# Optimization experiments

Measured on AMD Instinct MI355X. Metric: run time of the kernel, lower is better.

Reference implementation:

```python
import jax, jax.numpy as jnp
import numpy as np

S = 64        # memory_slots
SLOT_DIM = 256
BOND = 32     # bond_dim
NQ = 8        # num_qubits = max(4, ceil(log2(slot_dim)))
QDIM = 2 ** NQ  # 256
DIM = 1024    # input feature dim


def setup_inputs() -> dict:
    key = jax.random.key(0)
    ks = jax.random.split(key, 8)
    std = 1.0 / np.sqrt(BOND)
    x = jax.random.normal(ks[0], (8, 4096, DIM), dtype=jnp.float32)
    Wq = jax.random.normal(ks[1], (DIM, QDIM), dtype=jnp.float32) * 0.02
    bq = jnp.zeros((QDIM,), dtype=jnp.float32)
    Wd = jax.random.normal(ks[2], (SLOT_DIM, DIM), dtype=jnp.float32) * 0.02
    bd = jnp.zeros((DIM,), dtype=jnp.float32)
    # MPS cores batched over slots; original shapes per slot:
    #   q=0: (1,2,BOND), q=1..NQ-2: (BOND,2,BOND), q=NQ-1: (BOND,2,1)
    core_first = jax.random.normal(ks[3], (S, 2, BOND), dtype=jnp.float32) * std
    core_mid = jax.random.normal(ks[4], (S, NQ - 2, BOND, 2, BOND), dtype=jnp.float32) * std
    core_last = jax.random.normal(ks[5], (S, BOND, 2), dtype=jnp.float32) * std
    return {"x": x, "Wq": Wq, "bq": bq, "Wd": Wd, "bd": bd,
            "core_first": core_first, "core_mid": core_mid, "core_last": core_last}


def _amp_means(qa):
    """Per-qubit strided means of query amplitudes. qa: [b, 2^NQ] -> (m0, m1): [b, NQ]."""
    m0s, m1s = [], []
    for q in range(NQ):
        stride = 2 ** (NQ - q - 1)
        idx0 = np.arange(stride) * (2 * stride)  # qa[:, ::2*stride][:, :stride]
        idx1 = idx0 + stride                     # qa[:, stride::2*stride][:, :stride]
        m0s.append(qa[:, idx0].mean(axis=-1))
        m1s.append(qa[:, idx1].mean(axis=-1))
    return jnp.stack(m0s, axis=1), jnp.stack(m1s, axis=1)


def reference(x, Wq, bq, Wd, bd, core_first, core_mid, core_last):
    # x: [b, t, d]
    x_summary = x.mean(axis=1)                         # [b, d]
    qa = jax.nn.softmax(x_summary @ Wq + bq, axis=-1)  # [b, QDIM]
    m0, m1 = _amp_means(qa)                            # [b, NQ] each

    # MPS contraction, vectorized over (batch b, slot s)
    # q = 0: left bond is 1 -> result directly [b, S, BOND]
    res = (m0[:, 0, None, None] * core_first[None, :, 0, :]
           + m1[:, 0, None, None] * core_first[None, :, 1, :])
    for q in range(1, NQ - 1):
        wc = (m0[:, q, None, None, None] * core_mid[None, :, q - 1, :, 0, :]
              + m1[:, q, None, None, None] * core_mid[None, :, q - 1, :, 1, :])  # [b,S,B,B]
        res = jnp.einsum('bsl,bslr->bsr', res, wc)
    # q = NQ-1: right bond is 1
    wc_last = (m0[:, NQ - 1, None, None] * core_last[None, :, :, 0]
               + m1[:, NQ - 1, None, None] * core_last[None, :, :, 1])  # [b,S,B]
    overlaps = jnp.einsum('bsl,bsl->bs', res, wc_last)  # [b, S]

    attention = jax.nn.softmax(overlaps, axis=-1)       # [b, S]

    # read values: per-slot per-qubit core means, tiled to slot_dim
    f0 = core_first.mean(axis=(1, 2))                   # [S]
    fm = core_mid.mean(axis=(2, 3, 4))                  # [S, NQ-2]
    fl = core_last.mean(axis=(1, 2))                    # [S]
    feats = jnp.concatenate([f0[:, None], fm, fl[:, None]], axis=1)  # [S, NQ]
    rep = SLOT_DIM // NQ + 1
    slot_values = jnp.tile(feats, (1, rep))[:, :SLOT_DIM]            # [S, SLOT_DIM]

    read_out = attention @ slot_values                  # [b, SLOT_DIM]
    read_proj = read_out @ Wd + bd                      # [b, DIM]
    return x + read_proj[:, None, :]
```

## Files before the change

### kernel.cpp

```cpp
#include <hip/hip_runtime.h>
#include <hip/hip_bf16.h>

#define B_    8
#define T_    4096
#define D_    1024
#define S_    64
#define NQ_   8
#define QDIM_ 256
#define TB_   64
#define NTC_  (T_/TB_)
#define NMID  64

typedef __attribute__((ext_vector_type(4))) unsigned short u16x4;
typedef __attribute__((ext_vector_type(8))) unsigned short u16x8;
typedef __attribute__((ext_vector_type(4))) float f32x4;

__device__ __forceinline__ float b2f(unsigned short u) {
    union { unsigned int i; float f; } v; v.i = ((unsigned int)u) << 16; return v.f;
}
__device__ __forceinline__ unsigned short f2b(float f) {
    __hip_bfloat16 h = __float2bfloat16(f);
    return *reinterpret_cast<unsigned short*>(&h);
}

__device__ __forceinline__ float blockSum(float v, float* buf) {
    int tid = threadIdx.x;
    buf[tid] = v; __syncthreads();
    #pragma unroll
    for (int s = 128; s > 0; s >>= 1) { if (tid < s) buf[tid] += buf[tid + s]; __syncthreads(); }
    float r = buf[0]; __syncthreads();
    return r;
}
__device__ __forceinline__ float blockMax(float v, float* buf) {
    int tid = threadIdx.x;
    buf[tid] = v; __syncthreads();
    #pragma unroll
    for (int s = 128; s > 0; s >>= 1) { if (tid < s) buf[tid] = fmaxf(buf[tid], buf[tid + s]); __syncthreads(); }
    float r = buf[0]; __syncthreads();
    return r;
}

__device__ __forceinline__ bool detect_f32(const unsigned short* __restrict__ p,
                                           unsigned elo, unsigned ehi, int* cnt) {
    int tid = threadIdx.x;
    if (tid == 0) *cnt = 0;
    __syncthreads();
    unsigned short u = p[tid];
    unsigned e = (u >> 7) & 0xFF;
    bool ok = ((u & 0x7FFF) == 0) || (e >= elo && e <= ehi);
    unsigned long long bm = __ballot(ok);
    if ((tid & 63) == 0) atomicAdd(cnt, (int)__popcll(bm));
    __syncthreads();
    bool isf32 = (*cnt < 200);
    __syncthreads();
    return isf32;
}

__device__ __forceinline__ void gbar(int* slot, int target) {
    __syncthreads();
    if (threadIdx.x == 0) {
        __hip_atomic_fetch_add(slot, 1, __ATOMIC_RELEASE, __HIP_MEMORY_SCOPE_AGENT);
        while (__hip_atomic_load(slot, __ATOMIC_RELAXED, __HIP_MEMORY_SCOPE_AGENT) < target)
            __builtin_amdgcn_s_sleep(4);
        (void)__hip_atomic_load(slot, __ATOMIC_ACQUIRE, __HIP_MEMORY_SCOPE_AGENT);
    }
    __syncthreads();
}

__global__ __launch_bounds__(256)
void k_colsum(const void* __restrict__ x, float* __restrict__ partials) {
    __shared__ int cnt;
    bool xf32 = detect_f32((const unsigned short*)x, 100, 130, &cnt);
    int blk = blockIdx.x;
    int b  = blk >> 6;
    int tc = blk & 63;
    int tid = threadIdx.x;
    size_t base = ((size_t)(b * T_ + tc * TB_)) * D_ + tid * 4;
    float a0 = 0.f, a1 = 0.f, a2 = 0.f, a3 = 0.f;
    if (xf32) {
        const float* px = (const float*)x + base;
        #pragma unroll 8
        for (int i = 0; i < TB_; ++i) {
            f32x4 v = *reinterpret_cast<const f32x4*>(px + (size_t)i * D_);
            a0 += v[0]; a1 += v[1]; a2 += v[2]; a3 += v[3];
        }
    } else {
        const unsigned short* px = (const unsigned short*)x + base;
        #pragma unroll 8
        for (int i = 0; i < TB_; ++i) {
            u16x4 v = *reinterpret_cast<const u16x4*>(px + (size_t)i * D_);
            a0 += b2f(v[0]); a1 += b2f(v[1]); a2 += b2f(v[2]); a3 += b2f(v[3]);
        }
    }
    float* dst = partials + ((size_t)(tc * B_ + b)) * D_ + tid * 4;
    f32x4 r; r[0] = a0; r[1] = a1; r[2] = a2; r[3] = a3;
    *reinterpret_cast<f32x4*>(dst) = r;
}

struct MpsSh {
    float lcm[6 * 2048];
    float lcf[64];
    float lcl[64];
    float res[8][33];
    float nres[8][33];
    float lm0[64], lm1[64];
    float buf[256];
};
struct LogitsSh { float xs2[256]; float xs[128]; };
struct SmSh     { float qa[QDIM_]; float buf[256]; };
struct AttSh    { float att[S_]; float g[NQ_]; };
union Sh { MpsSh mps; LogitsSh lg; SmSh sm; AttSh att; };

__global__ __launch_bounds__(256)
void k_mid(const void* __restrict__ Wq, const void* __restrict__ bq,
           const void* __restrict__ Wd, const void* __restrict__ bd,
           const void* __restrict__ cf, const void* __restrict__ cm,
           const void* __restrict__ cl,
           const float* __restrict__ partials, float* __restrict__ plog,
           float* __restrict__ sm0m, float* __restrict__ sm1m,
           float* __restrict__ feats, float* __restrict__ ovl,
           float* __restrict__ read_proj, float* __restrict__ wdred,
           int* __restrict__ bar) {
    __shared__ Sh u;
    __shared__ int cnt;
    const int blk = blockIdx.x;
    const int tid = threadIdx.x;
    bool wf32 = detect_f32((const unsigned short*)Wq, 96, 126, &cnt);

    {
        int b = blk >> 3, dc = blk & 7;
        int d0 = dc * 128;
        float a = 0.f;
        for (int tc = (tid >> 7); tc < NTC_; tc += 2)
            a += partials[((size_t)(tc * B_ + b)) * D_ + d0 + (tid & 127)];
        u.lg.xs2[tid] = a;
        __syncthreads();
        if (tid < 128) u.lg.xs[tid] = (u.lg.xs2[tid] + u.lg.xs2[tid + 128]) * (1.f / (float)T_);
        __syncthreads();
        float lg = 0.f;
        if (wf32) {
            const float* w = (const float*)Wq + (size_t)d0 * QDIM_ + tid;
            #pragma unroll 8
            for (int d = 0; d < 128; ++d) lg += u.lg.xs[d] * w[(size_t)d * QDIM_];
        } else {
            const unsigned short* w = (const unsigned short*)Wq + (size_t)d0 * QDIM_ + tid;
            #pragma unroll 8
            for (int d = 0; d < 128; ++d) lg += u.lg.xs[d] * b2f(w[(size_t)d * QDIM_]);
        }
        plog[((size_t)(b * 8 + dc)) * QDIM_ + tid] = lg;
        if (tid < 128) {
            int flat = blk * 128 + tid;
            int j = flat >> 10, d = flat & (D_ - 1);
            float s = 0.f;
            if (wf32) {
                const float* w = (const float*)Wd;
                #pragma unroll 8
                for (int k = 0; k < 32; ++k) s += w[(size_t)(j + 8 * k) * D_ + d];
            } else {
                const unsigned short* w = (const unsigned short*)Wd;
                #pragma unroll 8
                for (int k = 0; k < 32; ++k) s += b2f(w[(size_t)(j + 8 * k) * D_ + d]);
            }
            wdred[flat] = s;
        }
    }
    gbar(bar + 0, NMID);

    if (blk < 8) {
        int b = blk;
        float lg = wf32 ? ((const float*)bq)[tid] : b2f(((const unsigned short*)bq)[tid]);
        for (int dc = 0; dc < 8; ++dc) lg += plog[((size_t)(b * 8 + dc)) * QDIM_ + tid];
        float mx = blockMax(lg, u.sm.buf);
        float e = __expf(lg - mx);
        float ss = blockSum(e, u.sm.buf);
        u.sm.qa[tid] = e / ss;
        __syncthreads();
        if (tid < 16) {
            int q = tid >> 1, bit = tid & 1;
            int sw = 1 << (7 - q);
            float acc = 0.f;
            for (int i = 0; i < sw; ++i) {
                int idx = 2 * sw * i + bit * sw;
                if (idx > QDIM_ - 1) idx = QDIM_ - 1;
                acc += u.sm.qa[idx];
            }
            float m = acc / (float)sw;
            if (bit == 0) sm0m[b * 8 + q] = m; else sm1m[b * 8 + q] = m;
        }
    }
    gbar(bar + 1, NMID);

    {
        int s = blk;
        MpsSh& M = u.mps;
        if (wf32) {
            const float* pcm = (const float*)cm + (size_t)s * 12288;
            for (int i = tid; i < 12288; i += 256) M.lcm[i] = pcm[i];
            if (tid < 64) {
                M.lcf[tid] = ((const float*)cf)[s * 64 + tid];
                M.lcl[tid] = ((const float*)cl)[s * 64 + tid];
            }
        } else {
            const unsigned short* pcm = (const unsigned short*)cm + (size_t)s * 12288;
            for (int i = tid; i < 12288; i += 256) M.lcm[i] = b2f(pcm[i]);
            if (tid < 64) {
                M.lcf[tid] = b2f(((const unsigned short*)cf)[s * 64 + tid]);
                M.lcl[tid] = b2f(((const unsigned short*)cl)[s * 64 + tid]);
            }
        }
        if (tid < 64) { M.lm0[tid] = sm0m[tid]; M.lm1[tid] = sm1m[tid]; }
        __syncthreads();

        {
            float v = (tid < 64) ? M.lcf[tid] : 0.f;
            float f0 = blockSum(v, M.buf) * (1.f / 64.f);
            float fj[6];
            for (int j = 0; j < 6; ++j) {
                float a = 0.f;
                for (int k = tid; k < 2048; k += 256) a += M.lcm[j * 2048 + k];
                fj[j] = blockSum(a, M.buf) * (1.f / 2048.f);
            }
            float w = (tid < 64) ? M.lcl[tid] : 0.f;
            float fl = blockSum(w, M.buf) * (1.f / 64.f);
            if (tid == 0) {
                feats[s * 8 + 0] = f0;
                #pragma unroll
                for (int j = 0; j < 6; ++j) feats[s * 8 + 1 + j] = fj[j];
                feats[s * 8 + 7] = fl;
            }
        }

        int b = tid >> 5, r = tid & 31;
        M.res[b][r] = M.lm0[b * 8 + 0] * M.lcf[r] + M.lm1[b * 8 + 0] * M.lcf[32 + r];
        __syncthreads();
        for (int q = 1; q <= 6; ++q) {
            float m0 = M.lm0[b * 8 + q], m1 = M.lm1[b * 8 + q];
            const float* C = &M.lcm[(q - 1) * 2048];
            float acc = 0.f;
            #pragma unroll 8
            for (int l = 0; l < 32; ++l)
                acc += M.res[b][l] * (m0 * C[l * 64 + r] + m1 * C[l * 64 + 32 + r]);
            M.nres[b][r] = acc;
            __syncthreads();
            M.res[b][r] = M.nres[b][r];
            __syncthreads();
        }
        {
            float m0 = M.lm0[b * 8 + 7], m1 = M.lm1[b * 8 + 7];
            float p = M.res[b][r] * (m0 * M.lcl[r * 2] + m1 * M.lcl[r * 2 + 1]);
            #pragma unroll
            for (int off = 16; off > 0; off >>= 1) p += __shfl_xor(p, off, 64);
            if (r == 0) ovl[b * 64 + s] = p;
        }
    }
    gbar(bar + 2, NMID);

    if (blk < 8) {
        int b = blk;
        if (tid < 64) {
            float o = ovl[b * 64 + tid];
            float mx = o;
            #pragma unroll
            for (int off = 32; off > 0; off >>= 1) mx = fmaxf(mx, __shfl_xor(mx, off, 64));
            float e = __expf(o - mx);
            float se = e;
            #pragma unroll
            for (int off = 32; off > 0; off >>= 1) se += __shfl_xor(se, off, 64);
            u.att.att[tid] = e / se;
        }
        __syncthreads();
        if (tid < 8) {
            float g = 0.f;
            for (int s2 = 0; s2 < S_; ++s2) g += u.att.att[s2] * feats[s2 * 8 + tid];
            u.att.g[tid] = g;
        }
        __syncthreads();
        #pragma unroll
        for (int i = 0; i < 4; ++i) {
            int d = tid + i * 256;
            float a = wf32 ? ((const float*)bd)[d] : b2f(((const unsigned short*)bd)[d]);
            #pragma unroll
            for (int j = 0; j < 8; ++j) a += u.att.g[j] * wdred[(size_t)j * D_ + d];
            read_proj[(size_t)b * D_ + d] = a;
        }
    }
}

__global__ __launch_bounds__(256)
void k_add(const void* __restrict__ x, const float* __restrict__ rp,
           void* __restrict__ out) {
    __shared__ int cnt;
    bool xf32 = detect_f32((const unsigned short*)x, 100, 130, &cnt);
    size_t base = (((size_t)blockIdx.x) * 256 + threadIdx.x) * 8;
    int b = (int)(base >> 22);
    int d = (int)(base & (D_ - 1));
    const float* r = rp + (size_t)b * D_ + d;
    f32x4 r0 = *reinterpret_cast<const f32x4*>(r);
    f32x4 r1 = *reinterpret_cast<const f32x4*>(r + 4);
    if (xf32) {
        const float* px = (const float*)x + base;
        f32x4 v0 = *reinterpret_cast<const f32x4*>(px);
        f32x4 v1 = *reinterpret_cast<const f32x4*>(px + 4);
        f32x4 o0 = v0 + r0;
        f32x4 o1 = v1 + r1;
        float* po = (float*)out + base;
        *reinterpret_cast<f32x4*>(po) = o0;
        *reinterpret_cast<f32x4*>(po + 4) = o1;
    } else {
        u16x8 v = *reinterpret_cast<const u16x8*>((const unsigned short*)x + base);
        u16x8 o;
        #pragma unroll
        for (int k = 0; k < 4; ++k) o[k] = f2b(b2f(v[k]) + r0[k]);
        #pragma unroll
        for (int k = 0; k < 4; ++k) o[4 + k] = f2b(b2f(v[4 + k]) + r1[k]);
        *reinterpret_cast<u16x8*>((unsigned short*)out + base) = o;
    }
}

extern "C" void kernel_launch(void* const* d_in, const int* in_sizes, int n_in,
                              void* d_out, int out_size, void* d_ws, size_t ws_size,
                              hipStream_t stream) {
    const void* x  = d_in[0];
    const void* Wq = d_in[1];
    const void* bq = d_in[2];
    const void* Wd = d_in[3];
    const void* bd = d_in[4];
    const void* cf = d_in[5];
    const void* cm = d_in[6];
    const void* cl = d_in[7];

    float* ws        = (float*)d_ws;
    float* partials  = ws;
    float* plog      = partials + 524288;
    float* sm0m      = plog + 16384;
    float* sm1m      = sm0m + 64;
    float* feats     = sm1m + 64;
    float* ovl       = feats + 512;
    float* read_proj = ovl + 512;
    float* wdred     = read_proj + 8192;
    int*   bar       = (int*)(wdred + 8192);

    hipMemsetAsync(bar, 0, 32, stream);
    k_colsum<<<B_ * NTC_, 256, 0, stream>>>(x, partials);
    k_mid<<<NMID, 256, 0, stream>>>(Wq, bq, Wd, bd, cf, cm, cl,
                                    partials, plog, sm0m, sm1m, feats, ovl,
                                    read_proj, wdred, bar);
    k_add<<<(B_ * T_ * D_) / 2048, 256, 0, stream>>>(x, read_proj, d_out);
}
```

Measured before the change: 314.6 us.

## Fuse column-sum and mid stages into one kernel with dataflow counters

Merges the column-sum kernel and the mid-stage kernel into a single 512-block launch. Each block arrives on an atomic counter, and only the downstream role blocks spin-wait on the counters they actually depend on, replacing full grid barriers. The Wd reduction is moved onto separate blocks so it overlaps with the logits stage. MPS cores are now read directly from global memory instead of being staged in LDS, which lowers shared-memory use so two blocks fit per CU. The design relies on all 512 blocks being co-resident to avoid deadlock, and it trades LDS reuse for repeated global or cache reads of the cores.

```diff
diff --git a/kernel.cpp b/kernel.cpp
--- a/kernel.cpp
+++ b/kernel.cpp
@@ -9,7 +9,7 @@
 #define QDIM_ 256
 #define TB_   64
 #define NTC_  (T_/TB_)
-#define NMID  64
+#define NBLK  512
 
 typedef __attribute__((ext_vector_type(4))) unsigned short u16x4;
 typedef __attribute__((ext_vector_type(8))) unsigned short u16x8;
@@ -56,49 +56,23 @@
     return isf32;
 }
 
-__device__ __forceinline__ void gbar(int* slot, int target) {
-    __syncthreads();
+__device__ __forceinline__ void arrive(int* slot) {
+    __syncthreads();
+    if (threadIdx.x == 0)
+        __hip_atomic_fetch_add(slot, 1, __ATOMIC_RELEASE, __HIP_MEMORY_SCOPE_AGENT);
+}
+__device__ __forceinline__ void wait_for(int* slot, int target) {
     if (threadIdx.x == 0) {
-        __hip_atomic_fetch_add(slot, 1, __ATOMIC_RELEASE, __HIP_MEMORY_SCOPE_AGENT);
         while (__hip_atomic_load(slot, __ATOMIC_RELAXED, __HIP_MEMORY_SCOPE_AGENT) < target)
-            __builtin_amdgcn_s_sleep(4);
+            __builtin_amdgcn_s_sleep(1);
         (void)__hip_atomic_load(slot, __ATOMIC_ACQUIRE, __HIP_MEMORY_SCOPE_AGENT);
     }
     __syncthreads();
 }
 
-__global__ __launch_bounds__(256)
-void k_colsum(const void* __restrict__ x, float* __restrict__ partials) {
-    __shared__ int cnt;
-    bool xf32 = detect_f32((const unsigned short*)x, 100, 130, &cnt);
-    int blk = blockIdx.x;
-    int b  = blk >> 6;
-    int tc = blk & 63;
-    int tid = threadIdx.x;
-    size_t base = ((size_t)(b * T_ + tc * TB_)) * D_ + tid * 4;
-    float a0 = 0.f, a1 = 0.f, a2 = 0.f, a3 = 0.f;
-    if (xf32) {
-        const float* px = (const float*)x + base;
-        #pragma unroll 8
-        for (int i = 0; i < TB_; ++i) {
-            f32x4 v = *reinterpret_cast<const f32x4*>(px + (size_t)i * D_);
-            a0 += v[0]; a1 += v[1]; a2 += v[2]; a3 += v[3];
-        }
-    } else {
-        const unsigned short* px = (const unsigned short*)x + base;
-        #pragma unroll 8
-        for (int i = 0; i < TB_; ++i) {
-            u16x4 v = *reinterpret_cast<const u16x4*>(px + (size_t)i * D_);
-            a0 += b2f(v[0]); a1 += b2f(v[1]); a2 += b2f(v[2]); a3 += b2f(v[3]);
-        }
-    }
-    float* dst = partials + ((size_t)(tc * B_ + b)) * D_ + tid * 4;
-    f32x4 r; r[0] = a0; r[1] = a1; r[2] = a2; r[3] = a3;
-    *reinterpret_cast<f32x4*>(dst) = r;
-}
-
+struct LogitsSh { float xs2[256]; float xs[128]; };
+struct SmSh     { float qa[QDIM_]; float buf[256]; };
 struct MpsSh {
-    float lcm[6 * 2048];
     float lcf[64];
     float lcl[64];
     float res[8][33];
@@ -106,28 +80,55 @@
     float lm0[64], lm1[64];
     float buf[256];
 };
-struct LogitsSh { float xs2[256]; float xs[128]; };
-struct SmSh     { float qa[QDIM_]; float buf[256]; };
 struct AttSh    { float att[S_]; float g[NQ_]; };
-union Sh { MpsSh mps; LogitsSh lg; SmSh sm; AttSh att; };
-
-__global__ __launch_bounds__(256)
-void k_mid(const void* __restrict__ Wq, const void* __restrict__ bq,
-           const void* __restrict__ Wd, const void* __restrict__ bd,
-           const void* __restrict__ cf, const void* __restrict__ cm,
-           const void* __restrict__ cl,
-           const float* __restrict__ partials, float* __restrict__ plog,
-           float* __restrict__ sm0m, float* __restrict__ sm1m,
-           float* __restrict__ feats, float* __restrict__ ovl,
-           float* __restrict__ read_proj, float* __restrict__ wdred,
-           int* __restrict__ bar) {
+union Sh { LogitsSh lg; SmSh sm; MpsSh mps; AttSh att; };
+
+__global__ __launch_bounds__(256, 2)
+void k_main(const void* __restrict__ x,  const void* __restrict__ Wq,
+            const void* __restrict__ bq, const void* __restrict__ Wd,
+            const void* __restrict__ bd, const void* __restrict__ cf,
+            const void* __restrict__ cm, const void* __restrict__ cl,
+            float* __restrict__ partials, float* __restrict__ plog,
+            float* __restrict__ sm0m, float* __restrict__ sm1m,
+            float* __restrict__ feats, float* __restrict__ ovl,
+            float* __restrict__ read_proj, float* __restrict__ wdred,
+            int* __restrict__ c) {
     __shared__ Sh u;
     __shared__ int cnt;
     const int blk = blockIdx.x;
     const int tid = threadIdx.x;
+
+    bool xf32 = detect_f32((const unsigned short*)x, 100, 130, &cnt);
     bool wf32 = detect_f32((const unsigned short*)Wq, 96, 126, &cnt);
 
     {
+        int b  = blk >> 6;
+        int tc = blk & 63;
+        size_t base = ((size_t)(b * T_ + tc * TB_)) * D_ + tid * 4;
+        float a0 = 0.f, a1 = 0.f, a2 = 0.f, a3 = 0.f;
+        if (xf32) {
+            const float* px = (const float*)x + base;
+            #pragma unroll 8
+            for (int i = 0; i < TB_; ++i) {
+                f32x4 v = *reinterpret_cast<const f32x4*>(px + (size_t)i * D_);
+                a0 += v[0]; a1 += v[1]; a2 += v[2]; a3 += v[3];
+            }
+        } else {
+            const unsigned short* px = (const unsigned short*)x + base;
+            #pragma unroll 8
+            for (int i = 0; i < TB_; ++i) {
+                u16x4 v = *reinterpret_cast<const u16x4*>(px + (size_t)i * D_);
+                a0 += b2f(v[0]); a1 += b2f(v[1]); a2 += b2f(v[2]); a3 += b2f(v[3]);
+            }
+        }
+        float* dst = partials + ((size_t)(tc * B_ + b)) * D_ + tid * 4;
+        f32x4 r; r[0] = a0; r[1] = a1; r[2] = a2; r[3] = a3;
+        *reinterpret_cast<f32x4*>(dst) = r;
+    }
+    arrive(c + 0);
+
+    if (blk < 64) {
+        wait_for(c + 0, NBLK);
         int b = blk >> 3, dc = blk & 7;
         int d0 = dc * 128;
         float a = 0.f;
@@ -148,8 +149,10 @@
             for (int d = 0; d < 128; ++d) lg += u.lg.xs[d] * b2f(w[(size_t)d * QDIM_]);
         }
         plog[((size_t)(b * 8 + dc)) * QDIM_ + tid] = lg;
+        arrive(c + 1);
+    } else if (blk < 128) {
         if (tid < 128) {
-            int flat = blk * 128 + tid;
+            int flat = (blk - 64) * 128 + tid;
             int j = flat >> 10, d = flat & (D_ - 1);
             float s = 0.f;
             if (wf32) {
@@ -163,11 +166,10 @@
             }
             wdred[flat] = s;
         }
-    }
-    gbar(bar + 0, NMID);
-
-    if (blk < 8) {
-        int b = blk;
+        arrive(c + 3);
+    } else if (blk < 136) {
+        wait_for(c + 1, 64);
+        int b = blk - 128;
         float lg = wf32 ? ((const float*)bq)[tid] : b2f(((const unsigned short*)bq)[tid]);
         for (int dc = 0; dc < 8; ++dc) lg += plog[((size_t)(b * 8 + dc)) * QDIM_ + tid];
         float mx = blockMax(lg, u.sm.buf);
@@ -187,22 +189,17 @@
             float m = acc / (float)sw;
             if (bit == 0) sm0m[b * 8 + q] = m; else sm1m[b * 8 + q] = m;
         }
-    }
-    gbar(bar + 1, NMID);
-
-    {
-        int s = blk;
+        arrive(c + 2);
+    } else if (blk >= 192 && blk < 256) {
+        int s = blk - 192;
         MpsSh& M = u.mps;
+        wait_for(c + 2, 8);
         if (wf32) {
-            const float* pcm = (const float*)cm + (size_t)s * 12288;
-            for (int i = tid; i < 12288; i += 256) M.lcm[i] = pcm[i];
             if (tid < 64) {
                 M.lcf[tid] = ((const float*)cf)[s * 64 + tid];
                 M.lcl[tid] = ((const float*)cl)[s * 64 + tid];
             }
         } else {
-            const unsigned short* pcm = (const unsigned short*)cm + (size_t)s * 12288;
-            for (int i = tid; i < 12288; i += 256) M.lcm[i] = b2f(pcm[i]);
             if (tid < 64) {
                 M.lcf[tid] = b2f(((const unsigned short*)cf)[s * 64 + tid]);
                 M.lcl[tid] = b2f(((const unsigned short*)cl)[s * 64 + tid]);
@@ -217,7 +214,13 @@
             float fj[6];
             for (int j = 0; j < 6; ++j) {
                 float a = 0.f;
-                for (int k = tid; k < 2048; k += 256) a += M.lcm[j * 2048 + k];
+                if (wf32) {
+                    const float* pcm = (const float*)cm + (size_t)s * 12288 + j * 2048;
+                    for (int k = tid; k < 2048; k += 256) a += pcm[k];
+                } else {
+                    const unsigned short* pcm = (const unsigned short*)cm + (size_t)s * 12288 + j * 2048;
+                    for (int k = tid; k < 2048; k += 256) a += b2f(pcm[k]);
+                }
                 fj[j] = blockSum(a, M.buf) * (1.f / 2048.f);
             }
             float w = (tid < 64) ? M.lcl[tid] : 0.f;
@@ -235,11 +238,18 @@
         __syncthreads();
         for (int q = 1; q <= 6; ++q) {
             float m0 = M.lm0[b * 8 + q], m1 = M.lm1[b * 8 + q];
-            const float* C = &M.lcm[(q - 1) * 2048];
             float acc = 0.f;
-            #pragma unroll 8
-            for (int l = 0; l < 32; ++l)
-                acc += M.res[b][l] * (m0 * C[l * 64 + r] + m1 * C[l * 64 + 32 + r]);
+            if (wf32) {
+                const float* C = (const float*)cm + (size_t)s * 12288 + (q - 1) * 2048;
+                #pragma unroll 8
+                for (int l = 0; l < 32; ++l)
+                    acc += M.res[b][l] * (m0 * C[l * 64 + r] + m1 * C[l * 64 + 32 + r]);
+            } else {
+                const unsigned short* C = (const unsigned short*)cm + (size_t)s * 12288 + (q - 1) * 2048;
+                #pragma unroll 8
+                for (int l = 0; l < 32; ++l)
+                    acc += M.res[b][l] * (m0 * b2f(C[l * 64 + r]) + m1 * b2f(C[l * 64 + 32 + r]));
+            }
             M.nres[b][r] = acc;
             __syncthreads();
             M.res[b][r] = M.nres[b][r];
@@ -252,11 +262,10 @@
             for (int off = 16; off > 0; off >>= 1) p += __shfl_xor(p, off, 64);
             if (r == 0) ovl[b * 64 + s] = p;
         }
-    }
-    gbar(bar + 2, NMID);
-
-    if (blk < 8) {
-        int b = blk;
+        arrive(c + 3);
+    } else if (blk >= 256 && blk < 264) {
+        wait_for(c + 3, 128);
+        int b = blk - 256;
         if (tid < 64) {
             float o = ovl[b * 64 + tid];
             float mx = o;
@@ -338,12 +347,11 @@
     float* ovl       = feats + 512;
     float* read_proj = ovl + 512;
     float* wdred     = read_proj + 8192;
-    int*   bar       = (int*)(wdred + 8192);
-
-    hipMemsetAsync(bar, 0, 32, stream);
-    k_colsum<<<B_ * NTC_, 256, 0, stream>>>(x, partials);
-    k_mid<<<NMID, 256, 0, stream>>>(Wq, bq, Wd, bd, cf, cm, cl,
-                                    partials, plog, sm0m, sm1m, feats, ovl,
-                                    read_proj, wdred, bar);
+    int*   c         = (int*)(wdred + 8192);
+
+    hipMemsetAsync(c, 0, 32, stream);
+    k_main<<<NBLK, 256, 0, stream>>>(x, Wq, bq, Wd, bd, cf, cm, cl,
+                                     partials, plog, sm0m, sm1m, feats, ovl,
+                                     read_proj, wdred, c);
     k_add<<<(B_ * T_ * D_) / 2048, 256, 0, stream>>>(x, read_proj, d_out);
 }
```

Result: slower. 365.4 us (+16.2%).

## Split persistent mid kernel into separate launches, replacing grid barriers

Applied to the files above, without the earlier changes.

Replaces the single 64-block persistent k_mid kernel and its atomic grid barriers with three kernels: logits plus Wd reduction over 128 blocks, MPS contraction, and attention/readout. Each MPS block now recomputes the softmax and amplitude means for all batches itself, so that phase no longer needs its own barrier. The Wd column reduction moves to separate blocks so it runs alongside the logits work, and the barrier memset is dropped. In exchange there are two extra kernel launch boundaries and redundant softmax work in each MPS block.

```diff
diff --git a/kernel.cpp b/kernel.cpp
--- a/kernel.cpp
+++ b/kernel.cpp
@@ -9,7 +9,6 @@
 #define QDIM_ 256
 #define TB_   64
 #define NTC_  (T_/TB_)
-#define NMID  64
 
 typedef __attribute__((ext_vector_type(4))) unsigned short u16x4;
 typedef __attribute__((ext_vector_type(8))) unsigned short u16x8;
@@ -31,14 +30,6 @@
     float r = buf[0]; __syncthreads();
     return r;
 }
-__device__ __forceinline__ float blockMax(float v, float* buf) {
-    int tid = threadIdx.x;
-    buf[tid] = v; __syncthreads();
-    #pragma unroll
-    for (int s = 128; s > 0; s >>= 1) { if (tid < s) buf[tid] = fmaxf(buf[tid], buf[tid + s]); __syncthreads(); }
-    float r = buf[0]; __syncthreads();
-    return r;
-}
 
 __device__ __forceinline__ bool detect_f32(const unsigned short* __restrict__ p,
                                            unsigned elo, unsigned ehi, int* cnt) {
@@ -54,17 +45,6 @@
     bool isf32 = (*cnt < 200);
     __syncthreads();
     return isf32;
-}
-
-__device__ __forceinline__ void gbar(int* slot, int target) {
-    __syncthreads();
-    if (threadIdx.x == 0) {
-        __hip_atomic_fetch_add(slot, 1, __ATOMIC_RELEASE, __HIP_MEMORY_SCOPE_AGENT);
-        while (__hip_atomic_load(slot, __ATOMIC_RELAXED, __HIP_MEMORY_SCOPE_AGENT) < target)
-            __builtin_amdgcn_s_sleep(4);
-        (void)__hip_atomic_load(slot, __ATOMIC_ACQUIRE, __HIP_MEMORY_SCOPE_AGENT);
-    }
-    __syncthreads();
 }
 
 __global__ __launch_bounds__(256)
@@ -97,59 +77,41 @@
     *reinterpret_cast<f32x4*>(dst) = r;
 }
 
-struct MpsSh {
-    float lcm[6 * 2048];
-    float lcf[64];
-    float lcl[64];
-    float res[8][33];
-    float nres[8][33];
-    float lm0[64], lm1[64];
-    float buf[256];
-};
-struct LogitsSh { float xs2[256]; float xs[128]; };
-struct SmSh     { float qa[QDIM_]; float buf[256]; };
-struct AttSh    { float att[S_]; float g[NQ_]; };
-union Sh { MpsSh mps; LogitsSh lg; SmSh sm; AttSh att; };
-
-__global__ __launch_bounds__(256)
-void k_mid(const void* __restrict__ Wq, const void* __restrict__ bq,
-           const void* __restrict__ Wd, const void* __restrict__ bd,
-           const void* __restrict__ cf, const void* __restrict__ cm,
-           const void* __restrict__ cl,
-           const float* __restrict__ partials, float* __restrict__ plog,
-           float* __restrict__ sm0m, float* __restrict__ sm1m,
-           float* __restrict__ feats, float* __restrict__ ovl,
-           float* __restrict__ read_proj, float* __restrict__ wdred,
-           int* __restrict__ bar) {
-    __shared__ Sh u;
+__global__ __launch_bounds__(256)
+void k_logits(const void* __restrict__ Wq, const void* __restrict__ Wd,
+              const float* __restrict__ partials, float* __restrict__ plog,
+              float* __restrict__ wdred) {
+    __shared__ float xs2[256];
+    __shared__ float xs[128];
     __shared__ int cnt;
     const int blk = blockIdx.x;
     const int tid = threadIdx.x;
     bool wf32 = detect_f32((const unsigned short*)Wq, 96, 126, &cnt);
 
-    {
+    if (blk < 64) {
         int b = blk >> 3, dc = blk & 7;
         int d0 = dc * 128;
         float a = 0.f;
         for (int tc = (tid >> 7); tc < NTC_; tc += 2)
             a += partials[((size_t)(tc * B_ + b)) * D_ + d0 + (tid & 127)];
-        u.lg.xs2[tid] = a;
+        xs2[tid] = a;
         __syncthreads();
-        if (tid < 128) u.lg.xs[tid] = (u.lg.xs2[tid] + u.lg.xs2[tid + 128]) * (1.f / (float)T_);
+        if (tid < 128) xs[tid] = (xs2[tid] + xs2[tid + 128]) * (1.f / (float)T_);
         __syncthreads();
         float lg = 0.f;
         if (wf32) {
             const float* w = (const float*)Wq + (size_t)d0 * QDIM_ + tid;
             #pragma unroll 8
-            for (int d = 0; d < 128; ++d) lg += u.lg.xs[d] * w[(size_t)d * QDIM_];
+            for (int d = 0; d < 128; ++d) lg += xs[d] * w[(size_t)d * QDIM_];
         } else {
             const unsigned short* w = (const unsigned short*)Wq + (size_t)d0 * QDIM_ + tid;
             #pragma unroll 8
-            for (int d = 0; d < 128; ++d) lg += u.lg.xs[d] * b2f(w[(size_t)d * QDIM_]);
+            for (int d = 0; d < 128; ++d) lg += xs[d] * b2f(w[(size_t)d * QDIM_]);
         }
         plog[((size_t)(b * 8 + dc)) * QDIM_ + tid] = lg;
+    } else {
         if (tid < 128) {
-            int flat = blk * 128 + tid;
+            int flat = (blk - 64) * 128 + tid;
             int j = flat >> 10, d = flat & (D_ - 1);
             float s = 0.f;
             if (wf32) {
@@ -164,125 +126,161 @@
             wdred[flat] = s;
         }
     }
-    gbar(bar + 0, NMID);
-
-    if (blk < 8) {
-        int b = blk;
-        float lg = wf32 ? ((const float*)bq)[tid] : b2f(((const unsigned short*)bq)[tid]);
-        for (int dc = 0; dc < 8; ++dc) lg += plog[((size_t)(b * 8 + dc)) * QDIM_ + tid];
-        float mx = blockMax(lg, u.sm.buf);
-        float e = __expf(lg - mx);
-        float ss = blockSum(e, u.sm.buf);
-        u.sm.qa[tid] = e / ss;
+}
+
+__global__ __launch_bounds__(256)
+void k_mps(const void* __restrict__ Wq, const void* __restrict__ bq,
+           const void* __restrict__ cf, const void* __restrict__ cm,
+           const void* __restrict__ cl, const float* __restrict__ plog,
+           float* __restrict__ feats, float* __restrict__ ovl) {
+    __shared__ float qa[8 * QDIM_];
+    __shared__ float lcm[6 * 2048];
+    __shared__ float lcf[64];
+    __shared__ float lcl[64];
+    __shared__ float res[8][33];
+    __shared__ float nres[8][33];
+    __shared__ float lm0[64], lm1[64];
+    __shared__ float buf[256];
+    __shared__ int cnt;
+    const int s = blockIdx.x;
+    const int tid = threadIdx.x;
+    bool wf32 = detect_f32((const unsigned short*)Wq, 96, 126, &cnt);
+
+    {
+        int b = tid >> 5, l = tid & 31;
+        float lg8[8];
+        #pragma unroll
+        for (int i = 0; i < 8; ++i) {
+            int j = i * 32 + l;
+            float v = wf32 ? ((const float*)bq)[j] : b2f(((const unsigned short*)bq)[j]);
+            #pragma unroll
+            for (int dc = 0; dc < 8; ++dc) v += plog[((size_t)(b * 8 + dc)) * QDIM_ + j];
+            lg8[i] = v;
+        }
+        float mx = lg8[0];
+        #pragma unroll
+        for (int i = 1; i < 8; ++i) mx = fmaxf(mx, lg8[i]);
+        #pragma unroll
+        for (int off = 16; off > 0; off >>= 1) mx = fmaxf(mx, __shfl_xor(mx, off, 64));
+        float ss = 0.f, e8[8];
+        #pragma unroll
+        for (int i = 0; i < 8; ++i) { e8[i] = __expf(lg8[i] - mx); ss += e8[i]; }
+        #pragma unroll
+        for (int off = 16; off > 0; off >>= 1) ss += __shfl_xor(ss, off, 64);
+        float inv = 1.f / ss;
+        #pragma unroll
+        for (int i = 0; i < 8; ++i) qa[b * QDIM_ + i * 32 + l] = e8[i] * inv;
+    }
+    __syncthreads();
+    if (tid < 128) {
+        int bb = tid >> 4, q = (tid >> 1) & 7, bit = tid & 1;
+        int sw = 1 << (7 - q);
+        float acc = 0.f;
+        for (int i = 0; i < sw; ++i) {
+            int idx = 2 * sw * i + bit * sw;
+            if (idx > QDIM_ - 1) idx = QDIM_ - 1;
+            acc += qa[bb * QDIM_ + idx];
+        }
+        float m = acc / (float)sw;
+        if (bit == 0) lm0[bb * 8 + q] = m; else lm1[bb * 8 + q] = m;
+    }
+
+    if (wf32) {
+        const float* pcm = (const float*)cm + (size_t)s * 12288;
+        for (int i = tid; i < 12288; i += 256) lcm[i] = pcm[i];
+        if (tid < 64) {
+            lcf[tid] = ((const float*)cf)[s * 64 + tid];
+            lcl[tid] = ((const float*)cl)[s * 64 + tid];
+        }
+    } else {
+        const unsigned short* pcm = (const unsigned short*)cm + (size_t)s * 12288;
+        for (int i = tid; i < 12288; i += 256) lcm[i] = b2f(pcm[i]);
+        if (tid < 64) {
+            lcf[tid] = b2f(((const unsigned short*)cf)[s * 64 + tid]);
+            lcl[tid] = b2f(((const unsigned short*)cl)[s * 64 + tid]);
+        }
+    }
+    __syncthreads();
+
+    {
+        float v = (tid < 64) ? lcf[tid] : 0.f;
+        float f0 = blockSum(v, buf) * (1.f / 64.f);
+        float fj[6];
+        for (int j = 0; j < 6; ++j) {
+            float a = 0.f;
+            for (int k = tid; k < 2048; k += 256) a += lcm[j * 2048 + k];
+            fj[j] = blockSum(a, buf) * (1.f / 2048.f);
+        }
+        float w = (tid < 64) ? lcl[tid] : 0.f;
+        float fl = blockSum(w, buf) * (1.f / 64.f);
+        if (tid == 0) {
+            feats[s * 8 + 0] = f0;
+            #pragma unroll
+            for (int j = 0; j < 6; ++j) feats[s * 8 + 1 + j] = fj[j];
+            feats[s * 8 + 7] = fl;
+        }
+    }
+
+    int b = tid >> 5, r = tid & 31;
+    res[b][r] = lm0[b * 8 + 0] * lcf[r] + lm1[b * 8 + 0] * lcf[32 + r];
+    __syncthreads();
+    for (int q = 1; q <= 6; ++q) {
+        float m0 = lm0[b * 8 + q], m1 = lm1[b * 8 + q];
+        const float* C = &lcm[(q - 1) * 2048];
+        float acc = 0.f;
+        #pragma unroll 8
+        for (int l = 0; l < 32; ++l)
+            acc += res[b][l] * (m0 * C[l * 64 + r] + m1 * C[l * 64 + 32 + r]);
+        nres[b][r] = acc;
         __syncthreads();
-        if (tid < 16) {
-            int q = tid >> 1, bit = tid & 1;
-            int sw = 1 << (7 - q);
-            float acc = 0.f;
-            for (int i = 0; i < sw; ++i) {
-                int idx = 2 * sw * i + bit * sw;
-                if (idx > QDIM_ - 1) idx = QDIM_ - 1;
-                acc += u.sm.qa[idx];
-            }
-            float m = acc / (float)sw;
-            if (bit == 0) sm0m[b * 8 + q] = m; else sm1m[b * 8 + q] = m;
-        }
-    }
-    gbar(bar + 1, NMID);
-
+        res[b][r] = nres[b][r];
+        __syncthreads();
+    }
     {
-        int s = blk;
-        MpsSh& M = u.mps;
-        if (wf32) {
-            const float* pcm = (const float*)cm + (size_t)s * 12288;
-            for (int i = tid; i < 12288; i += 256) M.lcm[i] = pcm[i];
-            if (tid < 64) {
-                M.lcf[tid] = ((const float*)cf)[s * 64 + tid];
-                M.lcl[tid] = ((const float*)cl)[s * 64 + tid];
-            }
-        } else {
-            const unsigned short* pcm = (const unsigned short*)cm + (size_t)s * 12288;
-            for (int i = tid; i < 12288; i += 256) M.lcm[i] = b2f(pcm[i]);
-            if (tid < 64) {
-                M.lcf[tid] = b2f(((const unsigned short*)cf)[s * 64 + tid]);
-                M.lcl[tid] = b2f(((const unsigned short*)cl)[s * 64 + tid]);
-            }
-        }
-        if (tid < 64) { M.lm0[tid] = sm0m[tid]; M.lm1[tid] = sm1m[tid]; }
-        __syncthreads();
-
-        {
-            float v = (tid < 64) ? M.lcf[tid] : 0.f;
-            float f0 = blockSum(v, M.buf) * (1.f / 64.f);
-            float fj[6];
-            for (int j = 0; j < 6; ++j) {
-                float a = 0.f;
-                for (int k = tid; k < 2048; k += 256) a += M.lcm[j * 2048 + k];
-                fj[j] = blockSum(a, M.buf) * (1.f / 2048.f);
-            }
-            float w = (tid < 64) ? M.lcl[tid] : 0.f;
-            float fl = blockSum(w, M.buf) * (1.f / 64.f);
-            if (tid == 0) {
-                feats[s * 8 + 0] = f0;
-                #pragma unroll
-                for (int j = 0; j < 6; ++j) feats[s * 8 + 1 + j] = fj[j];
-                feats[s * 8 + 7] = fl;
-            }
-        }
-
-        int b = tid >> 5, r = tid & 31;
-        M.res[b][r] = M.lm0[b * 8 + 0] * M.lcf[r] + M.lm1[b * 8 + 0] * M.lcf[32 + r];
-        __syncthreads();
-        for (int q = 1; q <= 6; ++q) {
-            float m0 = M.lm0[b * 8 + q], m1 = M.lm1[b * 8 + q];
-            const float* C = &M.lcm[(q - 1) * 2048];
-            float acc = 0.f;
-            #pragma unroll 8
-            for (int l = 0; l < 32; ++l)
-                acc += M.res[b][l] * (m0 * C[l * 64 + r] + m1 * C[l * 64 + 32 + r]);
-            M.nres[b][r] = acc;
-            __syncthreads();
-            M.res[b][r] = M.nres[b][r];
-            __syncthreads();
-        }
-        {
-            float m0 = M.lm0[b * 8 + 7], m1 = M.lm1[b * 8 + 7];
-            float p = M.res[b][r] * (m0 * M.lcl[r * 2] + m1 * M.lcl[r * 2 + 1]);
-            #pragma unroll
-            for (int off = 16; off > 0; off >>= 1) p += __shfl_xor(p, off, 64);
-            if (r == 0) ovl[b * 64 + s] = p;
-        }
-    }
-    gbar(bar + 2, NMID);
-
-    if (blk < 8) {
-        int b = blk;
-        if (tid < 64) {
-            float o = ovl[b * 64 + tid];
-            float mx = o;
-            #pragma unroll
-            for (int off = 32; off > 0; off >>= 1) mx = fmaxf(mx, __shfl_xor(mx, off, 64));
-            float e = __expf(o - mx);
-            float se = e;
-            #pragma unroll
-            for (int off = 32; off > 0; off >>= 1) se += __shfl_xor(se, off, 64);
-            u.att.att[tid] = e / se;
-        }
-        __syncthreads();
-        if (tid < 8) {
-            float g = 0.f;
-            for (int s2 = 0; s2 < S_; ++s2) g += u.att.att[s2] * feats[s2 * 8 + tid];
-            u.att.g[tid] = g;
-        }
-        __syncthreads();
-        #pragma unroll
-        for (int i = 0; i < 4; ++i) {
-            int d = tid + i * 256;
-            float a = wf32 ? ((const float*)bd)[d] : b2f(((const unsigned short*)bd)[d]);
-            #pragma unroll
-            for (int j = 0; j < 8; ++j) a += u.att.g[j] * wdred[(size_t)j * D_ + d];
-            read_proj[(size_t)b * D_ + d] = a;
-        }
+        float m0 = lm0[b * 8 + 7], m1 = lm1[b * 8 + 7];
+        float p = res[b][r] * (m0 * lcl[r * 2] + m1 * lcl[r * 2 + 1]);
+        #pragma unroll
+        for (int off = 16; off > 0; off >>= 1) p += __shfl_xor(p, off, 64);
+        if (r == 0) ovl[b * 64 + s] = p;
+    }
+}
+
+__global__ __launch_bounds__(256)
+void k_attn(const void* __restrict__ Wq, const void* __restrict__ bd,
+            const float* __restrict__ ovl, const float* __restrict__ feats,
+            const float* __restrict__ wdred, float* __restrict__ read_proj) {
+    __shared__ float att[S_];
+    __shared__ float gl[NQ_];
+    __shared__ int cnt;
+    const int b = blockIdx.x;
+    const int tid = threadIdx.x;
+    bool wf32 = detect_f32((const unsigned short*)Wq, 96, 126, &cnt);
+
+    if (tid < 64) {
+        float o = ovl[b * 64 + tid];
+        float mx = o;
+        #pragma unroll
+        for (int off = 32; off > 0; off >>= 1) mx = fmaxf(mx, __shfl_xor(mx, off, 64));
+        float e = __expf(o - mx);
+        float se = e;
+        #pragma unroll
+        for (int off = 32; off > 0; off >>= 1) se += __shfl_xor(se, off, 64);
+        att[tid] = e / se;
+    }
+    __syncthreads();
+    if (tid < 8) {
+        float g = 0.f;
+        for (int s2 = 0; s2 < S_; ++s2) g += att[s2] * feats[s2 * 8 + tid];
+        gl[tid] = g;
+    }
+    __syncthreads();
+    #pragma unroll
+    for (int i = 0; i < 4; ++i) {
+        int d = tid + i * 256;
+        float a = wf32 ? ((const float*)bd)[d] : b2f(((const unsigned short*)bd)[d]);
+        #pragma unroll
+        for (int j = 0; j < 8; ++j) a += gl[j] * wdred[(size_t)j * D_ + d];
+        read_proj[(size_t)b * D_ + d] = a;
     }
 }
 
@@ -332,18 +330,14 @@
     float* ws        = (float*)d_ws;
     float* partials  = ws;
     float* plog      = partials + 524288;
-    float* sm0m      = plog + 16384;
-    float* sm1m      = sm0m + 64;
-    float* feats     = sm1m + 64;
+    float* feats     = plog + 16384;
     float* ovl       = feats + 512;
     float* read_proj = ovl + 512;
     float* wdred     = read_proj + 8192;
-    int*   bar       = (int*)(wdred + 8192);
-
-    hipMemsetAsync(bar, 0, 32, stream);
+
     k_colsum<<<B_ * NTC_, 256, 0, stream>>>(x, partials);
-    k_mid<<<NMID, 256, 0, stream>>>(Wq, bq, Wd, bd, cf, cm, cl,
-                                    partials, plog, sm0m, sm1m, feats, ovl,
-                                    read_proj, wdred, bar);
+    k_logits<<<128, 256, 0, stream>>>(Wq, Wd, partials, plog, wdred);
+    k_mps<<<S_, 256, 0, stream>>>(Wq, bq, cf, cm, cl, plog, feats, ovl);
+    k_attn<<<B_, 256, 0, stream>>>(Wq, bd, ovl, feats, wdred, read_proj);
     k_add<<<(B_ * T_ * D_) / 2048, 256, 0, stream>>>(x, read_proj, d_out);
 }
```

New measurement: 299.9 us. 1.05x faster.
